# Kernel tuning notes

Measured on AMD Instinct MI355X. Metric: run time of the kernel, lower is better.

The kernel has to match this reference:

```python
import jax, jax.numpy as jnp
import numpy as np

N = 100000       # nodes
E = 1600000      # edges
EA = 7           # edge_attr_dim
H = 64           # hidden_dim
L = 32           # latent_dim
G = 512          # graphs in batch
C = 6            # num_classes


def _gin_conv(x, src, dst, edge_attr, We, be, W1, b1, W2, b2, eps):
    # GINE-style: message = relu(x_j + edge_proj), sum-aggregate at dst, then 2-layer MLP
    m = jax.nn.relu(x[src] + edge_attr @ We + be)            # [E, d_in]
    agg = jax.ops.segment_sum(m, dst, num_segments=x.shape[0])
    h = (1.0 + eps) * x + agg                                # [N, d_in]
    return jax.nn.relu(h @ W1 + b1) @ W2 + b2                # [N, H]


def setup_inputs() -> dict:
    key = jax.random.key(0)
    ks = jax.random.split(key, 24)
    s = 0.05
    inp = {
        "x": jax.random.normal(ks[0], (N,), jnp.float32),
        "edge_index": jax.random.randint(ks[1], (2, E), 0, N, jnp.int64),
        "edge_attr": jax.random.uniform(ks[2], (E, EA), jnp.float32),
        "batch": jnp.sort(jax.random.randint(ks[3], (N,), 0, G, jnp.int64)),
        # conv1 (input dim 1)
        "We1": jax.random.normal(ks[4], (EA, 1), jnp.float32) * s,
        "be1": jnp.zeros((1,), jnp.float32),
        "W11": jax.random.normal(ks[5], (1, H), jnp.float32) * s,
        "b11": jnp.zeros((H,), jnp.float32),
        "W12": jax.random.normal(ks[6], (H, H), jnp.float32) * s,
        "b12": jnp.zeros((H,), jnp.float32),
        "eps1": jnp.float32(0.0),
        # conv2 (input dim H)
        "We2": jax.random.normal(ks[7], (EA, H), jnp.float32) * s,
        "be2": jnp.zeros((H,), jnp.float32),
        "W21": jax.random.normal(ks[8], (H, H), jnp.float32) * s,
        "b21": jnp.zeros((H,), jnp.float32),
        "W22": jax.random.normal(ks[9], (H, H), jnp.float32) * s,
        "b22": jnp.zeros((H,), jnp.float32),
        "eps2": jnp.float32(0.0),
        # heads
        "Wmu": jax.random.normal(ks[10], (H, L), jnp.float32) * s,
        "bmu": jnp.zeros((L,), jnp.float32),
        "Wlv": jax.random.normal(ks[11], (H, L), jnp.float32) * s,
        "blv": jnp.zeros((L,), jnp.float32),
        "Wc": jax.random.normal(ks[12], (L, C), jnp.float32) * s,
        "bc": jnp.zeros((C,), jnp.float32),
    }
    return inp


def reference(x, edge_index, edge_attr, batch,
              We1, be1, W11, b11, W12, b12, eps1,
              We2, be2, W21, b21, W22, b22, eps2,
              Wmu, bmu, Wlv, blv, Wc, bc):
    src, dst = edge_index[0], edge_index[1]
    h = x.reshape(-1, 1)                                        # [N,1]
    h = jax.nn.relu(_gin_conv(h, src, dst, edge_attr, We1, be1, W11, b11, W12, b12, eps1))
    h = jax.nn.relu(_gin_conv(h, src, dst, edge_attr, We2, be2, W21, b21, W22, b22, eps2))
    mu = h @ Wmu + bmu                                          # [N,L]
    logvar = h @ Wlv + blv                                      # [N,L]
    # reparameterize (training path)
    noise = jax.random.normal(jax.random.key(42), mu.shape, mu.dtype)
    z = mu + noise * jnp.exp(0.5 * logvar)
    # global mean pool over graphs
    zsum = jax.ops.segment_sum(z, batch, num_segments=G)        # [G,L]
    cnt = jax.ops.segment_sum(jnp.ones((z.shape[0],), z.dtype), batch, num_segments=G)
    graph_emb = zsum / jnp.maximum(cnt, 1.0)[:, None]
    class_logits = graph_emb @ Wc + bc                          # [G,C]
    return (z, mu, logvar, class_logits)
```

## Files before the change

kernel.cpp:

```cpp
#include <hip/hip_runtime.h>
#include <stdint.h>

#define N_NODES 100000
#define N_EDGES 1600000
#define EAD 7
#define H 64
#define LAT 32
#define NG 512
#define NC 6

#define C1_NPB 32
#define C2_NPB 32
#define HD_NPB 64
#define NZ (N_NODES * LAT)
#define F4_PER_ARR (NZ / 4)

static_assert(N_NODES % C1_NPB == 0, "conv1_node grid exact");
static_assert(N_NODES % C2_NPB == 0, "conv2_node grid exact");

__device__ __forceinline__ void threefry2x32_42(uint32_t& x0, uint32_t& x1) {
    const uint32_t k0 = 0u, k1 = 42u;
    const uint32_t k2 = k0 ^ k1 ^ 0x1BD11BDAu;
    x0 += k0; x1 += k1;
#define TF_ROUND(r) { x0 += x1; x1 = (x1 << (r)) | (x1 >> (32 - (r))); x1 ^= x0; }
    TF_ROUND(13) TF_ROUND(15) TF_ROUND(26) TF_ROUND(6)
    x0 += k1; x1 += k2 + 1u;
    TF_ROUND(17) TF_ROUND(29) TF_ROUND(16) TF_ROUND(24)
    x0 += k2; x1 += k0 + 2u;
    TF_ROUND(13) TF_ROUND(15) TF_ROUND(26) TF_ROUND(6)
    x0 += k0; x1 += k1 + 3u;
    TF_ROUND(17) TF_ROUND(29) TF_ROUND(16) TF_ROUND(24)
    x0 += k1; x1 += k2 + 4u;
    TF_ROUND(13) TF_ROUND(15) TF_ROUND(26) TF_ROUND(6)
    x0 += k2; x1 += k0 + 5u;
#undef TF_ROUND
}

__device__ __forceinline__ float erfinv_f32(float x) {
    float w = -log1pf(-x * x);
    float p;
    if (w < 5.0f) {
        w = w - 2.5f;
        p = 2.81022636e-08f;
        p = fmaf(p, w, 3.43273939e-07f);
        p = fmaf(p, w, -3.5233877e-06f);
        p = fmaf(p, w, -4.39150654e-06f);
        p = fmaf(p, w, 0.00021858087f);
        p = fmaf(p, w, -0.00125372503f);
        p = fmaf(p, w, -0.00417768164f);
        p = fmaf(p, w, 0.246640727f);
        p = fmaf(p, w, 1.50140941f);
    } else {
        w = sqrtf(w) - 3.0f;
        p = -0.000200214257f;
        p = fmaf(p, w, 0.000100950558f);
        p = fmaf(p, w, 0.00134934322f);
        p = fmaf(p, w, -0.00367342844f);
        p = fmaf(p, w, 0.00573950773f);
        p = fmaf(p, w, -0.0076224613f);
        p = fmaf(p, w, 0.00943887047f);
        p = fmaf(p, w, 1.00167406f);
        p = fmaf(p, w, 2.83297682f);
    }
    return p * x;
}

__global__ void conv1_edge(const float* __restrict__ x, const int* __restrict__ src,
                           const int* __restrict__ dst, const float* __restrict__ ea,
                           const float* __restrict__ We1, const float* __restrict__ be1,
                           float* __restrict__ agg1) {
    int e = blockIdx.x * blockDim.x + threadIdx.x;
    if (e >= N_EDGES) return;
    float proj = be1[0];
#pragma unroll
    for (int k = 0; k < EAD; k++) proj = fmaf(ea[e * EAD + k], We1[k], proj);
    float m = x[src[e]] + proj;
    m = m > 0.0f ? m : 0.0f;
    atomicAdd(&agg1[dst[e]], m);
}

__global__ void conv1_node(const float* __restrict__ x, const float* __restrict__ agg1,
                           const float* __restrict__ W11, const float* __restrict__ b11,
                           const float* __restrict__ W12, const float* __restrict__ b12,
                           const float* __restrict__ eps1, float* __restrict__ hout) {
    __shared__ float sW12[H * H];
    __shared__ float st[4][H];
    int tid = threadIdx.x;
    for (int i = tid; i < H * H; i += 256) sW12[i] = W12[i];
    int sub = tid >> 6, lane = tid & 63;
    float eps = eps1[0];
    float w11 = W11[lane], bb11 = b11[lane], bb12 = b12[lane];
    __syncthreads();
#pragma unroll
    for (int it = 0; it < C1_NPB / 4; it++) {
        int n = blockIdx.x * C1_NPB + it * 4 + sub;
        float h1 = fmaf(eps, x[n], x[n]) + agg1[n];
        float t = fmaf(h1, w11, bb11);
        st[sub][lane] = t > 0.0f ? t : 0.0f;
        __syncthreads();
        float acc = bb12;
#pragma unroll
        for (int j = 0; j < H; j++) acc = fmaf(st[sub][j], sW12[j * H + lane], acc);
        hout[(size_t)n * H + lane] = acc > 0.0f ? acc : 0.0f;
        __syncthreads();
    }
}

__global__ void conv2_edge(const float* __restrict__ h, const int* __restrict__ src,
                           const int* __restrict__ dst, const float* __restrict__ ea,
                           const float* __restrict__ We2, const float* __restrict__ be2,
                           float* __restrict__ agg2) {
    int lane = threadIdx.x & 63;
    int e = (blockIdx.x * blockDim.x + threadIdx.x) >> 6;
    if (e >= N_EDGES) return;
    int s = src[e], d = dst[e];
    float proj = be2[lane];
#pragma unroll
    for (int k = 0; k < EAD; k++) proj = fmaf(ea[e * EAD + k], We2[k * H + lane], proj);
    float m = h[(size_t)s * H + lane] + proj;
    m = m > 0.0f ? m : 0.0f;
    atomicAdd(&agg2[(size_t)d * H + lane], m);
}

__global__ void conv2_node(const float* __restrict__ hin, const float* __restrict__ agg2,
                           const float* __restrict__ W21, const float* __restrict__ b21,
                           const float* __restrict__ W22, const float* __restrict__ b22,
                           const float* __restrict__ eps2, float* __restrict__ hout) {
    __shared__ float sW21[H * H], sW22[H * H];
    __shared__ float sh2[4][H], st[4][H];
    int tid = threadIdx.x;
    for (int i = tid; i < H * H; i += 256) { sW21[i] = W21[i]; sW22[i] = W22[i]; }
    int sub = tid >> 6, lane = tid & 63;
    float e = eps2[0];
    float bb21 = b21[lane], bb22 = b22[lane];
    __syncthreads();
#pragma unroll
    for (int it = 0; it < C2_NPB / 4; it++) {
        int n = blockIdx.x * C2_NPB + it * 4 + sub;
        float hv = hin[(size_t)n * H + lane];
        sh2[sub][lane] = fmaf(e, hv, hv) + agg2[(size_t)n * H + lane];
        __syncthreads();
        float acc = bb21;
#pragma unroll
        for (int j = 0; j < H; j++) acc = fmaf(sh2[sub][j], sW21[j * H + lane], acc);
        st[sub][lane] = acc > 0.0f ? acc : 0.0f;
        __syncthreads();
        acc = bb22;
#pragma unroll
        for (int j = 0; j < H; j++) acc = fmaf(st[sub][j], sW22[j * H + lane], acc);
        hout[(size_t)n * H + lane] = acc > 0.0f ? acc : 0.0f;
        __syncthreads();
    }
}

__global__ void heads_ml(const float* __restrict__ h,
                         const float* __restrict__ Wmu, const float* __restrict__ bmu,
                         const float* __restrict__ Wlv, const float* __restrict__ blv,
                         float* __restrict__ muws, float* __restrict__ lvws) {
    __shared__ float sWmu[H * LAT], sWlv[H * LAT];
    __shared__ float sh[8][H];
    int tid = threadIdx.x;
    for (int i = tid; i < H * LAT; i += 256) { sWmu[i] = Wmu[i]; sWlv[i] = Wlv[i]; }
    int sub = tid >> 5, lane = tid & 31;
    float bbmu = bmu[lane], bblv = blv[lane];
    __syncthreads();
    for (int it = 0; it < HD_NPB / 8; it++) {
        int base = blockIdx.x * HD_NPB + it * 8;
        if (base >= N_NODES) break;
        for (int i = tid; i < 8 * H; i += 256) {
            int nn = base + (i >> 6);
            if (nn < N_NODES) sh[i >> 6][i & 63] = h[(size_t)nn * H + (i & 63)];
        }
        __syncthreads();
        int n = base + sub;
        if (n < N_NODES) {
            float mu = bbmu, lv = bblv;
#pragma unroll
            for (int j = 0; j < H; j++) {
                float hv = sh[sub][j];
                mu = fmaf(hv, sWmu[j * LAT + lane], mu);
                lv = fmaf(hv, sWlv[j * LAT + lane], lv);
            }
            size_t o = (size_t)n * LAT + lane;
            muws[o] = mu; lvws[o] = lv;
        }
        __syncthreads();
    }
}

__global__ void heads_z(const float* __restrict__ muws, const float* __restrict__ lvws,
                        float* __restrict__ zws) {
    int i = blockIdx.x * blockDim.x + threadIdx.x;
    if (i >= NZ) return;
    float mu = muws[i], lv = lvws[i];
    uint32_t x0 = 0u, x1 = (uint32_t)i;
    threefry2x32_42(x0, x1);
    uint32_t bits = x0 ^ x1;
    float f = __uint_as_float((bits >> 9) | 0x3F800000u) - 1.0f;
    const float lo = -0.99999994f;
    float u = fmaxf(lo, fmaf(f, 2.0f, lo));
    float noise = 1.41421356237309515f * erfinv_f32(u);
    zws[i] = fmaf(noise, expf(0.5f * lv), mu);
}

__global__ void copyout_k(const float4* __restrict__ zs, const float4* __restrict__ ms,
                          const float4* __restrict__ ls, float4* __restrict__ out) {
    int i = blockIdx.x * blockDim.x + threadIdx.x;
    if (i < F4_PER_ARR) {
        out[i] = zs[i];
        out[F4_PER_ARR + i] = ms[i];
        out[2 * F4_PER_ARR + i] = ls[i];
    }
}

__global__ void pool_logits_k(const float4* __restrict__ z4, const int* __restrict__ batch,
                              const float* __restrict__ Wc, const float* __restrict__ bc,
                              float* __restrict__ out) {
    int g = blockIdx.x;
    int tid = threadIdx.x;
    int sub = tid >> 3, slot = tid & 7;
    __shared__ float4 acc4[32][8];
    __shared__ float emb[LAT];
    int lo = 0, hi = N_NODES;
    while (lo < hi) { int mid = (lo + hi) >> 1; if (batch[mid] < g) lo = mid + 1; else hi = mid; }
    int start = lo;
    hi = N_NODES;
    while (lo < hi) { int mid = (lo + hi) >> 1; if (batch[mid] < g + 1) lo = mid + 1; else hi = mid; }
    int end = lo;
    float4 a = make_float4(0.f, 0.f, 0.f, 0.f);
    for (int n = start + sub; n < end; n += 32) {
        float4 v = z4[(size_t)n * (LAT / 4) + slot];
        a.x += v.x; a.y += v.y; a.z += v.z; a.w += v.w;
    }
    acc4[sub][slot] = a;
    __syncthreads();
    if (tid < 8) {
        float4 s4 = acc4[0][tid];
        for (int k = 1; k < 32; k++) {
            s4.x += acc4[k][tid].x; s4.y += acc4[k][tid].y;
            s4.z += acc4[k][tid].z; s4.w += acc4[k][tid].w;
        }
        float invc = 1.0f / fmaxf((float)(end - start), 1.0f);
        emb[tid * 4 + 0] = s4.x * invc; emb[tid * 4 + 1] = s4.y * invc;
        emb[tid * 4 + 2] = s4.z * invc; emb[tid * 4 + 3] = s4.w * invc;
    }
    __syncthreads();
    if (tid < NC) {
        float r = bc[tid];
#pragma unroll
        for (int l = 0; l < LAT; l++) r = fmaf(emb[l], Wc[l * NC + tid], r);
        out[g * NC + tid] = r;
    }
}

extern "C" void kernel_launch(void* const* d_in, const int* in_sizes, int n_in,
                              void* d_out, int out_size, void* d_ws, size_t ws_size,
                              hipStream_t stream) {
    const float* x     = (const float*)d_in[0];
    const int*   ei    = (const int*)d_in[1];
    const float* ea    = (const float*)d_in[2];
    const int*   batch = (const int*)d_in[3];
    const float* We1   = (const float*)d_in[4];
    const float* be1   = (const float*)d_in[5];
    const float* W11   = (const float*)d_in[6];
    const float* b11   = (const float*)d_in[7];
    const float* W12   = (const float*)d_in[8];
    const float* b12   = (const float*)d_in[9];
    const float* eps1  = (const float*)d_in[10];
    const float* We2   = (const float*)d_in[11];
    const float* be2   = (const float*)d_in[12];
    const float* W21   = (const float*)d_in[13];
    const float* b21   = (const float*)d_in[14];
    const float* W22   = (const float*)d_in[15];
    const float* b22   = (const float*)d_in[16];
    const float* eps2  = (const float*)d_in[17];
    const float* Wmu   = (const float*)d_in[18];
    const float* bmu   = (const float*)d_in[19];
    const float* Wlv   = (const float*)d_in[20];
    const float* blv   = (const float*)d_in[21];
    const float* Wc    = (const float*)d_in[22];
    const float* bc    = (const float*)d_in[23];

    float* agg1 = (float*)d_ws;
    float* agg2 = agg1 + N_NODES;
    float* hA   = agg2 + (size_t)N_NODES * H;
    float* muws = agg2;
    float* lvws = agg2 + (size_t)NZ;
    float* zws  = hA;

    size_t zero_bytes = ((size_t)N_NODES + (size_t)N_NODES * H) * sizeof(float);
    hipMemsetAsync(d_ws, 0, zero_bytes, stream);

    const int* src = ei;
    const int* dst = ei + N_EDGES;

    conv1_edge<<<(N_EDGES + 255) / 256, 256, 0, stream>>>(x, src, dst, ea, We1, be1, agg1);
    conv1_node<<<N_NODES / C1_NPB, 256, 0, stream>>>(x, agg1, W11, b11, W12, b12, eps1, hA);
    conv2_edge<<<N_EDGES / 4, 256, 0, stream>>>(hA, src, dst, ea, We2, be2, agg2);
    conv2_node<<<N_NODES / C2_NPB, 256, 0, stream>>>(hA, agg2, W21, b21, W22, b22, eps2, hA);
    heads_ml<<<(N_NODES + HD_NPB - 1) / HD_NPB, 256, 0, stream>>>(
        hA, Wmu, bmu, Wlv, blv, muws, lvws);
    heads_z<<<(NZ + 255) / 256, 256, 0, stream>>>(muws, lvws, zws);
    copyout_k<<<(F4_PER_ARR + 255) / 256, 256, 0, stream>>>(
        (const float4*)zws, (const float4*)muws, (const float4*)lvws, (float4*)d_out);
    pool_logits_k<<<NG, 256, 0, stream>>>((const float4*)zws, batch, Wc, bc,
                                          (float*)d_out + 3 * (size_t)NZ);
}
```

Baseline: 766.7 us.

## Build dst-sorted CSR on device and fuse edge aggregation into node MLPs

```diff
diff --git a/kernel.cpp b/kernel.cpp
--- a/kernel.cpp
+++ b/kernel.cpp
@@ -9,14 +9,17 @@
 #define NG 512
 #define NC 6
 
-#define C1_NPB 32
-#define C2_NPB 32
+#define C1F 100
+#define C2F 100
 #define HD_NPB 64
 #define NZ (N_NODES * LAT)
 #define F4_PER_ARR (NZ / 4)
-
-static_assert(N_NODES % C1_NPB == 0, "conv1_node grid exact");
-static_assert(N_NODES % C2_NPB == 0, "conv2_node grid exact");
+#define NBLK ((N_NODES + 255) / 256)
+
+static_assert(N_NODES % C1F == 0 && C1F % 4 == 0, "conv1 grid exact");
+static_assert(N_NODES % C2F == 0 && C2F % 4 == 0, "conv2 grid exact");
+static_assert(N_EDGES % 256 == 0, "edge grid exact");
+static_assert(NBLK <= 512, "scan_partials capacity");
 
 __device__ __forceinline__ void threefry2x32_42(uint32_t& x0, uint32_t& x1) {
     const uint32_t k0 = 0u, k1 = 42u;
@@ -65,36 +68,97 @@
     return p * x;
 }
 
-__global__ void conv1_edge(const float* __restrict__ x, const int* __restrict__ src,
-                           const int* __restrict__ dst, const float* __restrict__ ea,
-                           const float* __restrict__ We1, const float* __restrict__ be1,
-                           float* __restrict__ agg1) {
+__global__ void csr_count(const int* __restrict__ dst, int* __restrict__ deg) {
     int e = blockIdx.x * blockDim.x + threadIdx.x;
-    if (e >= N_EDGES) return;
-    float proj = be1[0];
-#pragma unroll
-    for (int k = 0; k < EAD; k++) proj = fmaf(ea[e * EAD + k], We1[k], proj);
-    float m = x[src[e]] + proj;
-    m = m > 0.0f ? m : 0.0f;
-    atomicAdd(&agg1[dst[e]], m);
-}
-
-__global__ void conv1_node(const float* __restrict__ x, const float* __restrict__ agg1,
-                           const float* __restrict__ W11, const float* __restrict__ b11,
-                           const float* __restrict__ W12, const float* __restrict__ b12,
-                           const float* __restrict__ eps1, float* __restrict__ hout) {
+    if (e < N_EDGES) atomicAdd(&deg[dst[e]], 1);
+}
+
+__global__ void scan_bsums(const int* __restrict__ deg, int* __restrict__ bsum) {
+    __shared__ int s[256];
+    int t = threadIdx.x, i = blockIdx.x * 256 + t;
+    s[t] = (i < N_NODES) ? deg[i] : 0;
+    __syncthreads();
+    for (int off = 128; off > 0; off >>= 1) {
+        if (t < off) s[t] += s[t + off];
+        __syncthreads();
+    }
+    if (t == 0) bsum[blockIdx.x] = s[0];
+}
+
+__global__ void scan_partials(int* __restrict__ bsum) {
+    __shared__ int s[512];
+    int t = threadIdx.x;
+    int v = (t < NBLK) ? bsum[t] : 0;
+    s[t] = v;
+    __syncthreads();
+    for (int off = 1; off < 512; off <<= 1) {
+        int add = (t >= off) ? s[t - off] : 0;
+        __syncthreads();
+        s[t] += add;
+        __syncthreads();
+    }
+    if (t < NBLK) bsum[t] = s[t] - v;
+}
+
+__global__ void scan_base(const int* __restrict__ deg, const int* __restrict__ bsum,
+                          int* __restrict__ base) {
+    __shared__ int s[256];
+    int t = threadIdx.x, i = blockIdx.x * 256 + t;
+    int v = (i < N_NODES) ? deg[i] : 0;
+    s[t] = v;
+    __syncthreads();
+    for (int off = 1; off < 256; off <<= 1) {
+        int add = (t >= off) ? s[t - off] : 0;
+        __syncthreads();
+        s[t] += add;
+        __syncthreads();
+    }
+    if (i < N_NODES) base[i] = bsum[blockIdx.x] + s[t] - v;
+}
+
+__global__ void csr_fill(const int* __restrict__ dst, int* __restrict__ base,
+                         int* __restrict__ eids) {
+    int e = blockIdx.x * blockDim.x + threadIdx.x;
+    if (e < N_EDGES) {
+        int slot = atomicAdd(&base[dst[e]], 1);
+        eids[slot] = e;
+    }
+}
+
+__global__ void conv1_fused(const float* __restrict__ x, const int* __restrict__ src,
+                            const float* __restrict__ ea, const int* __restrict__ eids,
+                            const int* __restrict__ base, const int* __restrict__ deg,
+                            const float* __restrict__ We1, const float* __restrict__ be1,
+                            const float* __restrict__ W11, const float* __restrict__ b11,
+                            const float* __restrict__ W12, const float* __restrict__ b12,
+                            const float* __restrict__ eps1, float* __restrict__ hout) {
     __shared__ float sW12[H * H];
     __shared__ float st[4][H];
     int tid = threadIdx.x;
     for (int i = tid; i < H * H; i += 256) sW12[i] = W12[i];
     int sub = tid >> 6, lane = tid & 63;
-    float eps = eps1[0];
+    float eps = eps1[0], be1s = be1[0];
+    float we1r[EAD];
+#pragma unroll
+    for (int j = 0; j < EAD; j++) we1r[j] = We1[j];
     float w11 = W11[lane], bb11 = b11[lane], bb12 = b12[lane];
     __syncthreads();
-#pragma unroll
-    for (int it = 0; it < C1_NPB / 4; it++) {
-        int n = blockIdx.x * C1_NPB + it * 4 + sub;
-        float h1 = fmaf(eps, x[n], x[n]) + agg1[n];
+    for (int it = 0; it < C1F / 4; it++) {
+        int n = blockIdx.x * C1F + it * 4 + sub;
+        int cnt = deg[n], s0 = base[n] - cnt;
+        float part = 0.0f;
+        for (int k = lane; k < cnt; k += 64) {
+            int e = eids[s0 + k];
+            float proj = be1s;
+#pragma unroll
+            for (int j = 0; j < EAD; j++) proj = fmaf(ea[e * EAD + j], we1r[j], proj);
+            float m = x[src[e]] + proj;
+            part += fmaxf(m, 0.0f);
+        }
+#pragma unroll
+        for (int off = 1; off < 64; off <<= 1) part += __shfl_xor(part, off, 64);
+        float xn = x[n];
+        float h1 = fmaf(eps, xn, xn) + part;
         float t = fmaf(h1, w11, bb11);
         st[sub][lane] = t > 0.0f ? t : 0.0f;
         __syncthreads();
@@ -106,39 +170,39 @@
     }
 }
 
-__global__ void conv2_edge(const float* __restrict__ h, const int* __restrict__ src,
-                           const int* __restrict__ dst, const float* __restrict__ ea,
-                           const float* __restrict__ We2, const float* __restrict__ be2,
-                           float* __restrict__ agg2) {
-    int lane = threadIdx.x & 63;
-    int e = (blockIdx.x * blockDim.x + threadIdx.x) >> 6;
-    if (e >= N_EDGES) return;
-    int s = src[e], d = dst[e];
-    float proj = be2[lane];
-#pragma unroll
-    for (int k = 0; k < EAD; k++) proj = fmaf(ea[e * EAD + k], We2[k * H + lane], proj);
-    float m = h[(size_t)s * H + lane] + proj;
-    m = m > 0.0f ? m : 0.0f;
-    atomicAdd(&agg2[(size_t)d * H + lane], m);
-}
-
-__global__ void conv2_node(const float* __restrict__ hin, const float* __restrict__ agg2,
-                           const float* __restrict__ W21, const float* __restrict__ b21,
-                           const float* __restrict__ W22, const float* __restrict__ b22,
-                           const float* __restrict__ eps2, float* __restrict__ hout) {
+__global__ void conv2_fused(const float* __restrict__ hA, const int* __restrict__ src,
+                            const float* __restrict__ ea, const int* __restrict__ eids,
+                            const int* __restrict__ base, const int* __restrict__ deg,
+                            const float* __restrict__ We2, const float* __restrict__ be2,
+                            const float* __restrict__ W21, const float* __restrict__ b21,
+                            const float* __restrict__ W22, const float* __restrict__ b22,
+                            const float* __restrict__ eps2, float* __restrict__ hB) {
     __shared__ float sW21[H * H], sW22[H * H];
     __shared__ float sh2[4][H], st[4][H];
     int tid = threadIdx.x;
     for (int i = tid; i < H * H; i += 256) { sW21[i] = W21[i]; sW22[i] = W22[i]; }
     int sub = tid >> 6, lane = tid & 63;
-    float e = eps2[0];
-    float bb21 = b21[lane], bb22 = b22[lane];
-    __syncthreads();
-#pragma unroll
-    for (int it = 0; it < C2_NPB / 4; it++) {
-        int n = blockIdx.x * C2_NPB + it * 4 + sub;
-        float hv = hin[(size_t)n * H + lane];
-        sh2[sub][lane] = fmaf(e, hv, hv) + agg2[(size_t)n * H + lane];
+    float epsv = eps2[0];
+    float we2r[EAD];
+#pragma unroll
+    for (int j = 0; j < EAD; j++) we2r[j] = We2[j * H + lane];
+    float be2r = be2[lane], bb21 = b21[lane], bb22 = b22[lane];
+    __syncthreads();
+    for (int it = 0; it < C2F / 4; it++) {
+        int n = blockIdx.x * C2F + it * 4 + sub;
+        int cnt = deg[n], s0 = base[n] - cnt;
+        float agg = 0.0f;
+        for (int k = 0; k < cnt; k++) {
+            int e = eids[s0 + k];
+            int s = src[e];
+            float proj = be2r;
+#pragma unroll
+            for (int j = 0; j < EAD; j++) proj = fmaf(ea[e * EAD + j], we2r[j], proj);
+            float m = hA[(size_t)s * H + lane] + proj;
+            agg += fmaxf(m, 0.0f);
+        }
+        float hv = hA[(size_t)n * H + lane];
+        sh2[sub][lane] = fmaf(epsv, hv, hv) + agg;
         __syncthreads();
         float acc = bb21;
 #pragma unroll
@@ -148,7 +212,7 @@
         acc = bb22;
 #pragma unroll
         for (int j = 0; j < H; j++) acc = fmaf(st[sub][j], sW22[j * H + lane], acc);
-        hout[(size_t)n * H + lane] = acc > 0.0f ? acc : 0.0f;
+        hB[(size_t)n * H + lane] = acc > 0.0f ? acc : 0.0f;
         __syncthreads();
     }
 }
@@ -281,25 +345,34 @@
     const float* Wc    = (const float*)d_in[22];
     const float* bc    = (const float*)d_in[23];
 
-    float* agg1 = (float*)d_ws;
-    float* agg2 = agg1 + N_NODES;
-    float* hA   = agg2 + (size_t)N_NODES * H;
-    float* muws = agg2;
-    float* lvws = agg2 + (size_t)NZ;
-    float* zws  = hA;
-
-    size_t zero_bytes = ((size_t)N_NODES + (size_t)N_NODES * H) * sizeof(float);
-    hipMemsetAsync(d_ws, 0, zero_bytes, stream);
+    float* hB   = (float*)d_ws;
+    float* hA   = hB + (size_t)N_NODES * H;
+    int*   deg  = (int*)(hA + (size_t)N_NODES * H);
+    int*   base = deg + N_NODES;
+    int*   bsum = base + N_NODES;
+    int*   eids = (int*)d_out;
+    float* muws = hA;
+    float* lvws = hA + (size_t)NZ;
+    float* zws  = hB;
+
+    hipMemsetAsync(deg, 0, N_NODES * sizeof(int), stream);
 
     const int* src = ei;
     const int* dst = ei + N_EDGES;
 
-    conv1_edge<<<(N_EDGES + 255) / 256, 256, 0, stream>>>(x, src, dst, ea, We1, be1, agg1);
-    conv1_node<<<N_NODES / C1_NPB, 256, 0, stream>>>(x, agg1, W11, b11, W12, b12, eps1, hA);
-    conv2_edge<<<N_EDGES / 4, 256, 0, stream>>>(hA, src, dst, ea, We2, be2, agg2);
-    conv2_node<<<N_NODES / C2_NPB, 256, 0, stream>>>(hA, agg2, W21, b21, W22, b22, eps2, hA);
+    csr_count<<<N_EDGES / 256, 256, 0, stream>>>(dst, deg);
+    scan_bsums<<<NBLK, 256, 0, stream>>>(deg, bsum);
+    scan_partials<<<1, 512, 0, stream>>>(bsum);
+    scan_base<<<NBLK, 256, 0, stream>>>(deg, bsum, base);
+    csr_fill<<<N_EDGES / 256, 256, 0, stream>>>(dst, base, eids);
+
+    conv1_fused<<<N_NODES / C1F, 256, 0, stream>>>(x, src, ea, eids, base, deg,
+                                                   We1, be1, W11, b11, W12, b12, eps1, hA);
+    conv2_fused<<<N_NODES / C2F, 256, 0, stream>>>(hA, src, ea, eids, base, deg,
+                                                   We2, be2, W21, b21, W22, b22, eps2, hB);
+
     heads_ml<<<(N_NODES + HD_NPB - 1) / HD_NPB, 256, 0, stream>>>(
-        hA, Wmu, bmu, Wlv, blv, muws, lvws);
+        hB, Wmu, bmu, Wlv, blv, muws, lvws);
     heads_z<<<(NZ + 255) / 256, 256, 0, stream>>>(muws, lvws, zws);
     copyout_k<<<(F4_PER_ARR + 255) / 256, 256, 0, stream>>>(
         (const float4*)zws, (const float4*)muws, (const float4*)lvws, (float4*)d_out);
```

After: 995.1 us. 1.3x slower.
